# Performance work log

Measured on AMD Instinct MI355X. Metric: run time of the kernel, lower is better.

## Reference

```python
import jax, jax.numpy as jnp
import numpy as np

BETA = 0.25
NUM_EMBEDDINGS = 512
DIM_EMBEDDING = 64


def setup_inputs() -> dict:
    key = jax.random.key(0)
    k1, k2 = jax.random.split(key)
    z_e = jax.random.normal(k1, (32, 64, 64, 64), dtype=jnp.float32)
    # torch init: uniform_(-1/num_embeddings, 1/num_embeddings)
    lim = 1.0 / NUM_EMBEDDINGS
    embeddings = jax.random.uniform(
        k2, (NUM_EMBEDDINGS, DIM_EMBEDDING), dtype=jnp.float32,
        minval=-lim, maxval=lim)
    return {"z_e": z_e, "embeddings": embeddings}


def reference(z_e, embeddings):
    # Flatten exactly as torch's z_e.view(-1, dim_embedding) on (N,C,H,W)
    z_flat = z_e.reshape(-1, DIM_EMBEDDING)          # [M, D]
    # Squared euclidean distances: ||z||^2 + ||e||^2 - 2 z e^T
    distances = (
        jnp.sum(z_flat ** 2, axis=1, keepdims=True)
        + jnp.sum(embeddings ** 2, axis=1)
        - 2.0 * jnp.matmul(z_flat, embeddings.T)
    )                                                # [M, K]
    encoding_indices = jnp.argmin(distances, axis=1)[:, None]  # [M, 1]
    quantized = embeddings[encoding_indices[:, 0]].reshape(z_e.shape)
    # Straight-through estimator
    quantized_st = z_e + jax.lax.stop_gradient(quantized - z_e)
    recon_loss = jnp.mean((jax.lax.stop_gradient(quantized_st) - z_e) ** 2)
    commitment_loss = BETA * jnp.mean(
        (quantized_st - jax.lax.stop_gradient(z_e)) ** 2)
    loss = recon_loss + commitment_loss
    return (loss, quantized_st, encoding_indices)
```

## Files before the change

### kernel.cpp

```cpp
#include <hip/hip_runtime.h>
#include <hip/hip_bf16.h>

constexpr int NELEM = 8388608;
constexpr int ROWS  = 64;
constexpr int TPB   = 4;
constexpr int NBLK  = 131072 / ROWS / TPB;
constexpr int ZS    = 68;
constexpr float EPS = 1e-3f;
constexpr int QCAP  = 1024;

typedef short bf16x8 __attribute__((ext_vector_type(8)));
typedef float v4f    __attribute__((ext_vector_type(4)));

__device__ bf16x8 g_efrag[32][2][64];
__device__ float  g_en2[512];

__device__ inline bf16x8 cvt_hi8(const float* __restrict__ s, float scale) {
    bf16x8 h;
#pragma unroll
    for (int j = 0; j < 8; ++j) {
        __hip_bfloat16 b = __float2bfloat16(scale * s[j]);
        h[j] = (short)__bfloat16_as_ushort(b);
    }
    return h;
}

__global__ void __launch_bounds__(256) vq_prep(const float* __restrict__ emb,
                                               float* __restrict__ out) {
    const int b = blockIdx.x;
    if (b < 16) {
        const int id   = b * 256 + threadIdx.x;
        const int lane = id & 63;
        const int kc   = (id >> 6) & 1;
        const int ct   = id >> 7;
        const float* src = emb + (size_t)(ct * 16 + (lane & 15)) * 64
                               + kc * 32 + (lane >> 4) * 8;
        g_efrag[ct][kc][lane] = cvt_hi8(src, -2.0f);
    } else {
#pragma unroll
        for (int c = 0; c < 2; ++c) {
            const int k = threadIdx.x + c * 256;
            const float4* e4 = (const float4*)(emb + (size_t)k * 64);
            float a = 0.f, bq = 0.f, cc = 0.f, d = 0.f;
#pragma unroll
            for (int i = 0; i < 16; ++i) {
                float4 v = e4[i];
                a += v.x * v.x; bq += v.y * v.y; cc += v.z * v.z; d += v.w * v.w;
            }
            g_en2[k] = (a + bq) + (cc + d);
        }
        if (threadIdx.x == 0) out[0] = 0.f;
    }
}

__global__ __launch_bounds__(256) __attribute__((amdgpu_waves_per_eu(2, 2)))
void vq_main(const float* __restrict__ z,
             const float* __restrict__ emb,
             float* __restrict__ out) {
    __shared__ float s_z[ROWS * ZS];
    __shared__ float s_en2[512];
    __shared__ float s_zn2[ROWS];
    __shared__ unsigned long long s_key[ROWS];
    __shared__ float s_wmin[ROWS][4];
    __shared__ float s_thr[ROWS];
    __shared__ unsigned s_q[QCAP];
    __shared__ int s_qn;
    __shared__ float s_lpart[4];

    const int tid  = threadIdx.x;
    const int lane = tid & 63;
    const int wid  = __builtin_amdgcn_readfirstlane(tid >> 6);
    const int mcol = lane & 15;
    const int quad = lane >> 4;
    const int row4 = tid >> 2, seg4 = tid & 3;

    s_en2[tid]       = g_en2[tid];
    s_en2[tid + 256] = g_en2[tid + 256];
    {
        const float4* gp = (const float4*)(z +
            ((size_t)blockIdx.x * TPB * ROWS + row4) * 64 + seg4 * 16);
#pragma unroll
        for (int i = 0; i < 4; ++i)
            *(float4*)&s_z[row4 * ZS + seg4 * 16 + i * 4] = gp[i];
    }
    if (tid < ROWS) s_key[tid] = ~0ULL;
    if (tid == 0) s_qn = 0;
    __syncthreads();

    for (int t = 0; t < TPB; ++t) {
        const size_t tbase = (size_t)(blockIdx.x * TPB + t) * ROWS;

        float4 pf0, pf1, pf2, pf3;
        if (t + 1 < TPB) {
            const float4* gp = (const float4*)(z +
                (tbase + ROWS + row4) * 64 + seg4 * 16);
            pf0 = gp[0]; pf1 = gp[1]; pf2 = gp[2]; pf3 = gp[3];
        }

        {
            const float* zr = &s_z[row4 * ZS];
            float p = 0.f;
#pragma unroll
            for (int i = 0; i < 16; ++i) p += zr[4 * i + seg4] * zr[4 * i + seg4];
            p += __shfl_xor(p, 1, 64);
            p += __shfl_xor(p, 2, 64);
            if (seg4 == 0) s_zn2[row4] = p;
        }

        bf16x8 zf[4][2];
#pragma unroll
        for (int rg = 0; rg < 4; ++rg) {
            zf[rg][0] = cvt_hi8(&s_z[(rg * 16 + mcol) * ZS +  0 + quad * 8], 1.0f);
            zf[rg][1] = cvt_hi8(&s_z[(rg * 16 + mcol) * ZS + 32 + quad * 8], 1.0f);
        }

        float lmin[4];
#pragma unroll
        for (int rg = 0; rg < 4; ++rg) lmin[rg] = 3.402823466e38f;
#pragma unroll 2
        for (int ct = 0; ct < 8; ++ct) {
            const int gct = wid * 8 + ct;
            bf16x8 e0 = g_efrag[gct][0][lane];
            bf16x8 e1 = g_efrag[gct][1][lane];
            v4f base = *(const v4f*)&s_en2[gct * 16 + quad * 4];
#pragma unroll
            for (int rg = 0; rg < 4; ++rg) {
                v4f a = base;
                a = __builtin_amdgcn_mfma_f32_16x16x32_bf16(e0, zf[rg][0], a, 0, 0, 0);
                a = __builtin_amdgcn_mfma_f32_16x16x32_bf16(e1, zf[rg][1], a, 0, 0, 0);
                lmin[rg] = fminf(lmin[rg], fminf(fminf(a.x, a.y), fminf(a.z, a.w)));
            }
        }

#pragma unroll
        for (int rg = 0; rg < 4; ++rg) {
            float m = lmin[rg];
            m = fminf(m, __shfl_xor(m, 16, 64));
            m = fminf(m, __shfl_xor(m, 32, 64));
            if (quad == 0) s_wmin[rg * 16 + mcol][wid] = m;
        }
        __syncthreads();
        if (tid < ROWS)
            s_thr[tid] = fminf(fminf(s_wmin[tid][0], s_wmin[tid][1]),
                               fminf(s_wmin[tid][2], s_wmin[tid][3])) + EPS;
        __syncthreads();

        float thr[4];
#pragma unroll
        for (int rg = 0; rg < 4; ++rg) thr[rg] = s_thr[rg * 16 + mcol];
#pragma unroll 2
        for (int ct = 0; ct < 8; ++ct) {
            const int gct = wid * 8 + ct;
            bf16x8 e0 = g_efrag[gct][0][lane];
            bf16x8 e1 = g_efrag[gct][1][lane];
            v4f base = *(const v4f*)&s_en2[gct * 16 + quad * 4];
#pragma unroll
            for (int rg = 0; rg < 4; ++rg) {
                v4f a = base;
                a = __builtin_amdgcn_mfma_f32_16x16x32_bf16(e0, zf[rg][0], a, 0, 0, 0);
                a = __builtin_amdgcn_mfma_f32_16x16x32_bf16(e1, zf[rg][1], a, 0, 0, 0);
                float m4 = fminf(fminf(a.x, a.y), fminf(a.z, a.w));
                if (m4 <= thr[rg]) {
#pragma unroll
                    for (int r = 0; r < 4; ++r) {
                        if (a[r] <= thr[rg]) {
                            int slot = atomicAdd(&s_qn, 1);
                            if (slot < QCAP)
                                s_q[slot] = ((unsigned)(rg * 16 + mcol) << 16) |
                                            (unsigned)(wid * 128 + ct * 16 + quad * 4 + r);
                        }
                    }
                }
            }
        }
        __syncthreads();

        {
            const int qn = s_qn;
            for (int i = tid; i < qn && i < QCAP; i += 256) {
                const unsigned e = s_q[i];
                const int row = e >> 16, code = e & 0xFFFF;
                const float* zr = &s_z[row * ZS];
                const float* er = emb + (size_t)code * 64;
                float a = 0.f, b = 0.f, c2 = 0.f, d = 0.f;
#pragma unroll
                for (int g = 0; g < 16; ++g) {
                    a  += zr[4*g]   * er[4*g];   b += zr[4*g+1] * er[4*g+1];
                    c2 += zr[4*g+2] * er[4*g+2]; d += zr[4*g+3] * er[4*g+3];
                }
                float dot  = (a + b) + (c2 + d);
                float dist = (s_zn2[row] + s_en2[code]) - 2.0f * dot;
                unsigned long long key =
                    ((unsigned long long)__float_as_uint(dist) << 32) | (unsigned)code;
                atomicMin(&s_key[row], key);
            }
        }
        __syncthreads();

        {
            const int widx = (int)(unsigned)(s_key[row4] & 0x1FFULL);
            const float* er = emb + (size_t)widx * 64 + seg4 * 16;
            const float* zr = &s_z[row4 * ZS + seg4 * 16];
            float* qo = out + 1 + (tbase + row4) * 64 + seg4 * 16;
            float lsum = 0.f;
#pragma unroll
            for (int j = 0; j < 16; ++j) {
                float zv = zr[j], ev = er[j];
                float q = zv + (ev - zv);
                float df = q - zv; lsum += df * df;
                qo[j] = q;
            }
            if (seg4 == 0)
                out[1 + NELEM + tbase + row4] = (float)widx;

#pragma unroll
            for (int off = 32; off; off >>= 1) lsum += __shfl_down(lsum, off, 64);
            if (lane == 0) s_lpart[wid] = lsum;
        }
        __syncthreads();

        if (tid == 0) {
            float p = (s_lpart[0] + s_lpart[1]) + (s_lpart[2] + s_lpart[3]);
            atomicAdd(out, p * (1.25f / 8388608.0f));
            s_qn = 0;
        }
        if (tid < ROWS) s_key[tid] = ~0ULL;
        if (t + 1 < TPB) {
            float* d = &s_z[row4 * ZS + seg4 * 16];
            *(float4*)&d[0]  = pf0;  *(float4*)&d[4]  = pf1;
            *(float4*)&d[8]  = pf2;  *(float4*)&d[12] = pf3;
        }
        __syncthreads();
    }
}

extern "C" void kernel_launch(void* const* d_in, const int* in_sizes, int n_in,
                              void* d_out, int out_size, void* d_ws, size_t ws_size,
                              hipStream_t stream) {
    const float* z   = (const float*)d_in[0];
    const float* emb = (const float*)d_in[1];
    float* out = (float*)d_out;

    vq_prep<<<17, 256, 0, stream>>>(emb, out);
    vq_main<<<NBLK, 256, 0, stream>>>(z, emb, out);
}
```

Baseline: 138.0 us.

## Keep MFMA distance tiles in registers and stage codebook fragments in LDS

```diff
diff --git a/kernel.cpp b/kernel.cpp
--- a/kernel.cpp
+++ b/kernel.cpp
@@ -3,7 +3,7 @@
 
 constexpr int NELEM = 8388608;
 constexpr int ROWS  = 64;
-constexpr int TPB   = 4;
+constexpr int TPB   = 8;
 constexpr int NBLK  = 131072 / ROWS / TPB;
 constexpr int ZS    = 68;
 constexpr float EPS = 1e-3f;
@@ -53,10 +53,11 @@
     }
 }
 
-__global__ __launch_bounds__(256) __attribute__((amdgpu_waves_per_eu(2, 2)))
+__global__ __launch_bounds__(256) __attribute__((amdgpu_waves_per_eu(1, 1)))
 void vq_main(const float* __restrict__ z,
              const float* __restrict__ emb,
              float* __restrict__ out) {
+    __shared__ bf16x8 s_e[32][2][64];
     __shared__ float s_z[ROWS * ZS];
     __shared__ float s_en2[512];
     __shared__ float s_zn2[ROWS];
@@ -74,6 +75,11 @@
     const int quad = lane >> 4;
     const int row4 = tid >> 2, seg4 = tid & 3;
 
+#pragma unroll
+    for (int i = 0; i < 16; ++i) {
+        const int idx = tid + 256 * i;
+        ((bf16x8*)s_e)[idx] = ((const bf16x8*)g_efrag)[idx];
+    }
     s_en2[tid]       = g_en2[tid];
     s_en2[tid + 256] = g_en2[tid + 256];
     {
@@ -87,13 +93,15 @@
     if (tid == 0) s_qn = 0;
     __syncthreads();
 
+    float lacc = 0.f;
+
+#pragma unroll 1
     for (int t = 0; t < TPB; ++t) {
-        const size_t tbase = (size_t)(blockIdx.x * TPB + t) * ROWS;
+        const size_t tb = (size_t)(blockIdx.x * TPB + t) * ROWS;
 
         float4 pf0, pf1, pf2, pf3;
         if (t + 1 < TPB) {
-            const float4* gp = (const float4*)(z +
-                (tbase + ROWS + row4) * 64 + seg4 * 16);
+            const float4* gp = (const float4*)(z + (tb + ROWS + row4) * 64 + seg4 * 16);
             pf0 = gp[0]; pf1 = gp[1]; pf2 = gp[2]; pf3 = gp[3];
         }
 
@@ -114,20 +122,22 @@
             zf[rg][1] = cvt_hi8(&s_z[(rg * 16 + mcol) * ZS + 32 + quad * 8], 1.0f);
         }
 
+        v4f acc[4][8];
         float lmin[4];
 #pragma unroll
         for (int rg = 0; rg < 4; ++rg) lmin[rg] = 3.402823466e38f;
-#pragma unroll 2
+#pragma unroll
         for (int ct = 0; ct < 8; ++ct) {
             const int gct = wid * 8 + ct;
-            bf16x8 e0 = g_efrag[gct][0][lane];
-            bf16x8 e1 = g_efrag[gct][1][lane];
+            bf16x8 e0 = s_e[gct][0][lane];
+            bf16x8 e1 = s_e[gct][1][lane];
             v4f base = *(const v4f*)&s_en2[gct * 16 + quad * 4];
 #pragma unroll
             for (int rg = 0; rg < 4; ++rg) {
                 v4f a = base;
                 a = __builtin_amdgcn_mfma_f32_16x16x32_bf16(e0, zf[rg][0], a, 0, 0, 0);
                 a = __builtin_amdgcn_mfma_f32_16x16x32_bf16(e1, zf[rg][1], a, 0, 0, 0);
+                acc[rg][ct] = a;
                 lmin[rg] = fminf(lmin[rg], fminf(fminf(a.x, a.y), fminf(a.z, a.w)));
             }
         }
@@ -145,25 +155,17 @@
                                fminf(s_wmin[tid][2], s_wmin[tid][3])) + EPS;
         __syncthreads();
 
-        float thr[4];
-#pragma unroll
-        for (int rg = 0; rg < 4; ++rg) thr[rg] = s_thr[rg * 16 + mcol];
-#pragma unroll 2
-        for (int ct = 0; ct < 8; ++ct) {
-            const int gct = wid * 8 + ct;
-            bf16x8 e0 = g_efrag[gct][0][lane];
-            bf16x8 e1 = g_efrag[gct][1][lane];
-            v4f base = *(const v4f*)&s_en2[gct * 16 + quad * 4];
-#pragma unroll
-            for (int rg = 0; rg < 4; ++rg) {
-                v4f a = base;
-                a = __builtin_amdgcn_mfma_f32_16x16x32_bf16(e0, zf[rg][0], a, 0, 0, 0);
-                a = __builtin_amdgcn_mfma_f32_16x16x32_bf16(e1, zf[rg][1], a, 0, 0, 0);
+#pragma unroll
+        for (int rg = 0; rg < 4; ++rg) {
+            const float thr = s_thr[rg * 16 + mcol];
+#pragma unroll
+            for (int ct = 0; ct < 8; ++ct) {
+                v4f a = acc[rg][ct];
                 float m4 = fminf(fminf(a.x, a.y), fminf(a.z, a.w));
-                if (m4 <= thr[rg]) {
+                if (m4 <= thr) {
 #pragma unroll
                     for (int r = 0; r < 4; ++r) {
-                        if (a[r] <= thr[rg]) {
+                        if (a[r] <= thr) {
                             int slot = atomicAdd(&s_qn, 1);
                             if (slot < QCAP)
                                 s_q[slot] = ((unsigned)(rg * 16 + mcol) << 16) |
@@ -201,7 +203,7 @@
             const int widx = (int)(unsigned)(s_key[row4] & 0x1FFULL);
             const float* er = emb + (size_t)widx * 64 + seg4 * 16;
             const float* zr = &s_z[row4 * ZS + seg4 * 16];
-            float* qo = out + 1 + (tbase + row4) * 64 + seg4 * 16;
+            float* qo = out + 1 + (tb + row4) * 64 + seg4 * 16;
             float lsum = 0.f;
 #pragma unroll
             for (int j = 0; j < 16; ++j) {
@@ -211,26 +213,27 @@
                 qo[j] = q;
             }
             if (seg4 == 0)
-                out[1 + NELEM + tbase + row4] = (float)widx;
-
+                out[1 + NELEM + tb + row4] = (float)widx;
 #pragma unroll
             for (int off = 32; off; off >>= 1) lsum += __shfl_down(lsum, off, 64);
-            if (lane == 0) s_lpart[wid] = lsum;
-        }
-        __syncthreads();
-
-        if (tid == 0) {
-            float p = (s_lpart[0] + s_lpart[1]) + (s_lpart[2] + s_lpart[3]);
-            atomicAdd(out, p * (1.25f / 8388608.0f));
-            s_qn = 0;
-        }
-        if (tid < ROWS) s_key[tid] = ~0ULL;
+            if (lane == 0) lacc += lsum;
+            if (tid == 0) s_qn = 0;
+        }
+
+        if (lane < 16) s_key[wid * 16 + lane] = ~0ULL;
         if (t + 1 < TPB) {
             float* d = &s_z[row4 * ZS + seg4 * 16];
             *(float4*)&d[0]  = pf0;  *(float4*)&d[4]  = pf1;
             *(float4*)&d[8]  = pf2;  *(float4*)&d[12] = pf3;
         }
         __syncthreads();
+    }
+
+    if (lane == 0) s_lpart[wid] = lacc;
+    __syncthreads();
+    if (tid == 0) {
+        float p = (s_lpart[0] + s_lpart[1]) + (s_lpart[2] + s_lpart[3]);
+        atomicAdd(out, p * (1.25f / 8388608.0f));
     }
 }
 
```

Result: slower. 150.1 us (+8.8%).
